# Optimization experiments

Measured on AMD Instinct MI355X. Metric: run time of the kernel, lower is better.

Reference implementation:

```python
import jax, jax.numpy as jnp
import numpy as np

PI = 3.1415926
MAX_V = 8  # max vertices of a quad-quad convex intersection
ALPHA, GAMMA, IOU_THRES = 0.25, 2.0, 0.5


def xyxy2xywh_a(b):
    cx = (b[..., 0] + b[..., 2]) * 0.5
    cy = (b[..., 1] + b[..., 3]) * 0.5
    w = b[..., 2] - b[..., 0]
    h = b[..., 3] - b[..., 1]
    return jnp.stack([cx, cy, w, h, b[..., 4]], -1)


def rbox_2_quad(b):
    # [N,5] (x1,y1,x2,y2,theta_deg) -> [N,4,2] corner quads
    x = xyxy2xywh_a(b)
    cx, cy, w, h, t = x[:, 0], x[:, 1], x[:, 2], x[:, 3], x[:, 4]
    th = t * (PI / 180.0)
    c, s = jnp.cos(th), jnp.sin(th)
    dx = jnp.array([-0.5, 0.5, 0.5, -0.5], b.dtype)
    dy = jnp.array([-0.5, -0.5, 0.5, 0.5], b.dtype)
    px = cx[:, None] + dx * w[:, None] * c[:, None] - dy * h[:, None] * s[:, None]
    py = cy[:, None] + dx * w[:, None] * s[:, None] + dy * h[:, None] * c[:, None]
    return jnp.stack([px, py], -1)


def min_area_square(b):
    cx = (b[:, 0] + b[:, 2]) * 0.5
    cy = (b[:, 1] + b[:, 3]) * 0.5
    s = jnp.maximum(b[:, 2] - b[:, 0], b[:, 3] - b[:, 1]) * 0.5
    return jnp.stack([cx - s, cy - s, cx + s, cy + s], 1)


def bbox_overlaps(a, b):
    # axis-aligned IoU matrix [N,M]
    lt = jnp.maximum(a[:, None, :2], b[None, :, :2])
    rb = jnp.minimum(a[:, None, 2:], b[None, :, 2:])
    wh = jnp.clip(rb - lt, 0.0)
    inter = wh[..., 0] * wh[..., 1]
    area_a = (a[:, 2] - a[:, 0]) * (a[:, 3] - a[:, 1])
    area_b = (b[:, 2] - b[:, 0]) * (b[:, 3] - b[:, 1])
    return inter / (area_a[:, None] + area_b[None, :] - inter + 1e-6)


def points_in_quads(pts, quads):
    # pointsJf: pts [A,2] inside convex quads [G,4,2] -> [A,G] {0,1}
    e = jnp.roll(quads, -1, axis=1) - quads  # [G,4,2]
    rel = pts[:, None, None, :] - quads[None]  # [A,G,4,2]
    cr = e[None, ..., 0] * rel[..., 1] - e[None, ..., 1] * rel[..., 0]
    inside = jnp.all(cr >= 0, -1) | jnp.all(cr <= 0, -1)
    return inside.astype(pts.dtype)


def _signed_area2(q):
    return jnp.sum(q[:, 0] * jnp.roll(q[:, 1], -1) - jnp.roll(q[:, 0], -1) * q[:, 1])


def _quad_inter_area(q1, q2):
    # Sutherland-Hodgman clipping of quad q1 by convex quad q2, fixed 8-vertex buffer
    q1 = jnp.where(_signed_area2(q1) < 0, q1[::-1], q1)
    q2 = jnp.where(_signed_area2(q2) < 0, q2[::-1], q2)
    poly = jnp.zeros((MAX_V, 2), q1.dtype).at[:4].set(q1)
    edges = jnp.stack([q2, jnp.roll(q2, -1, axis=0)], 1)  # [4,2,2]

    def clip(carry, edge):
        poly, n = carry
        a, b = edge[0], edge[1]
        idx = jnp.arange(MAX_V)
        nidx = jnp.where(idx + 1 < n, idx + 1, 0)
        cur, nxt = poly, poly[nidx]
        d = b - a
        dc = d[0] * (cur[:, 1] - a[1]) - d[1] * (cur[:, 0] - a[0])
        dn = d[0] * (nxt[:, 1] - a[1]) - d[1] * (nxt[:, 0] - a[0])
        denom = dc - dn
        t = dc / jnp.where(jnp.abs(denom) < 1e-12, 1e-12, denom)
        inter = cur + t[:, None] * (nxt - cur)
        active = idx < n
        keep_cur = active & (dc >= 0)
        keep_int = active & ((dc >= 0) != (dn >= 0))
        pts = jnp.stack([cur, inter], 1).reshape(2 * MAX_V, 2)
        flags = jnp.stack([keep_cur, keep_int], 1).reshape(-1)
        pos = jnp.where(flags, jnp.cumsum(flags) - 1, MAX_V)
        newpoly = jnp.zeros((MAX_V + 1, 2), poly.dtype).at[pos].set(pts)[:MAX_V]
        return (newpoly, flags.sum()), None

    (poly, n), _ = jax.lax.scan(clip, (poly, jnp.int32(4)), edges)
    idx = jnp.arange(MAX_V)
    nidx = jnp.where(idx + 1 < n, idx + 1, 0)
    contrib = poly[:, 0] * poly[nidx, 1] - poly[nidx, 0] * poly[:, 1]
    area = 0.5 * jnp.abs(jnp.sum(jnp.where(idx < n, contrib, 0.0)))
    return jnp.where(n >= 3, area, 0.0)


def rbox_overlaps(quads_a, quads_g, gate, thresh=0.1):
    area_a = 0.5 * jnp.abs(jax.vmap(_signed_area2)(quads_a))
    area_g = 0.5 * jnp.abs(jax.vmap(_signed_area2)(quads_g))
    inter = jax.vmap(lambda qa: jax.vmap(lambda qg: _quad_inter_area(qa, qg))(quads_g))(quads_a)
    iou = inter / (area_a[:, None] + area_g[None, :] - inter + 1e-6)
    return jnp.where(gate > thresh, iou, 0.0)


def encode(anchors, gt):
    a = xyxy2xywh_a(anchors)
    g = xyxy2xywh_a(gt)
    dx = (g[:, 0] - a[:, 0]) / a[:, 2]
    dy = (g[:, 1] - a[:, 1]) / a[:, 3]
    dw = jnp.log(g[:, 2] / a[:, 2])
    dh = jnp.log(g[:, 3] / a[:, 3])
    dt = (g[:, 4] - a[:, 4]) * (PI / 180.0)
    return jnp.stack([dx, dy, dw, dh, dt], 1)


def decode(anchors, deltas):
    a = xyxy2xywh_a(anchors)
    cx = a[..., 0] + deltas[..., 0] * a[..., 2]
    cy = a[..., 1] + deltas[..., 1] * a[..., 3]
    w = a[..., 2] * jnp.exp(deltas[..., 2])
    h = a[..., 3] * jnp.exp(deltas[..., 3])
    t = a[..., 4] + deltas[..., 4] * (180.0 / PI)
    return jnp.stack([cx, cy, w, h, t], -1)


def smooth_l1(x, t, beta=1.0 / 9):
    diff = jnp.abs(x - t)
    return jnp.where(diff < beta, 0.5 * diff * diff / beta, diff - 0.5 * beta)


def _forward(classifications, regressions, anchors, annotations):
    B = classifications.shape[0]
    _ = decode(anchors, regressions)  # all_pred_boxes (unused when func='smooth')
    cls_losses, reg_losses = [], []
    for j in range(B):
        cls = jnp.clip(classifications[j], 1e-4, 1.0 - 1e-4)
        anch = anchors[j]
        gtb = annotations[j, :, :5]
        labels = annotations[j, :, 5].astype(jnp.int32)
        indicator = bbox_overlaps(min_area_square(anch), min_area_square(gtb))
        centers = xyxy2xywh_a(anch)[:, :2]
        quads_g = rbox_2_quad(gtb)
        inside = points_in_quads(centers, quads_g)
        quads_a = rbox_2_quad(anch)
        ious = rbox_overlaps(quads_a, quads_g, inside * indicator)  # [A,G]
        iou_max = ious.max(1)
        iou_argmax = ious.argmax(1)
        pos = iou_max >= IOU_THRES
        max_gt = ious.max(0)
        argmax_gt = ious.argmax(0)
        low = (max_gt < IOU_THRES).astype(jnp.int32)
        pos = (pos.astype(jnp.int32).at[argmax_gt].max(low)).astype(bool)
        num_pos = pos.sum()
        C = cls.shape[1]
        onehot = jax.nn.one_hot(labels[iou_argmax], C, dtype=cls.dtype)
        tgt = -jnp.ones_like(cls)
        tgt = jnp.where((iou_max < IOU_THRES - 0.1)[:, None], 0.0, tgt)
        tgt = jnp.where(pos[:, None], onehot, tgt)
        af = jnp.where(tgt == 1.0, ALPHA, 1.0 - ALPHA)
        fw = af * jnp.where(tgt == 1.0, 1.0 - cls, cls) ** GAMMA
        bce = -(tgt * jnp.log(cls + 1e-6) + (1.0 - tgt) * jnp.log(1.0 - cls + 1e-6))
        cls_loss = jnp.where(tgt != -1.0, fw * bce, 0.0).sum() / jnp.maximum(num_pos.astype(cls.dtype), 1.0)
        cls_losses.append(cls_loss)
        reg_t = encode(anch, gtb[iou_argmax])
        l = smooth_l1(regressions[j], reg_t)
        denom = (jnp.maximum(num_pos, 1) * l.shape[1]).astype(l.dtype)
        reg_loss = jnp.where(num_pos > 0, (l * pos[:, None].astype(l.dtype)).sum() / denom, 0.0)
        reg_losses.append(reg_loss)
    loss_cls = 5.0 * jnp.stack(cls_losses).mean(keepdims=True)
    loss_reg = 2.0 * jnp.stack(reg_losses).mean(keepdims=True)
    return loss_cls, loss_reg


def setup_inputs() -> dict:
    key = jax.random.key(0)
    ks = jax.random.split(key, 8)
    B, A, G, C = 2, 32768, 32, 15
    cls = jax.random.uniform(ks[0], (B, A, C), jnp.float32)
    reg = jax.random.normal(ks[1], (B, A, 5), jnp.float32) * 0.1
    ac = jax.random.uniform(ks[2], (B, A, 2), jnp.float32, 0.0, 1024.0)
    awh = jax.random.uniform(ks[3], (B, A, 2), jnp.float32, 16.0, 256.0)
    anchors = jnp.concatenate([ac - awh * 0.5, ac + awh * 0.5, jnp.zeros((B, A, 1), jnp.float32)], -1)
    gc = jax.random.uniform(ks[4], (B, G, 2), jnp.float32, 64.0, 960.0)
    gwh = jax.random.uniform(ks[5], (B, G, 2), jnp.float32, 24.0, 300.0)
    gt = jax.random.uniform(ks[6], (B, G, 1), jnp.float32, -90.0, 90.0)
    glab = jax.random.randint(ks[7], (B, G, 1), 0, C).astype(jnp.float32)
    annotations = jnp.concatenate([gc - gwh * 0.5, gc + gwh * 0.5, gt, glab], -1)
    return {"classifications": cls, "regressions": reg, "anchors": anchors, "annotations": annotations}


def reference(classifications, regressions, anchors, annotations):
    return _forward(classifications, regressions, anchors, annotations)
```

## Files before the change

### kernel.cpp

```cpp
#include <hip/hip_runtime.h>

#define A_N 32768
#define G_N 32
#define C_N 15
#define BPB 128
#define DEG2RAD ((float)(3.1415926 / 180.0))
#define BETA (1.0f / 9.0f)

typedef unsigned long long ull;

template <int NIN>
__device__ __forceinline__ int clip_pass(float ax, float ay, float dx, float dy,
                                         float (&PX)[8], float (&PY)[8], int n) {
  constexpr int NOUT = (NIN + 1 < 8) ? NIN + 1 : 8;
  float d[NIN];
#pragma unroll
  for (int i = 0; i < NIN; ++i)
    d[i] = dx * (PY[i] - ay) - dy * (PX[i] - ax);
  float NX[NOUT], NY[NOUT];
#pragma unroll
  for (int i = 0; i < NOUT; ++i) { NX[i] = 0.f; NY[i] = 0.f; }
  int m = 0;
#pragma unroll
  for (int i = 0; i < NIN; ++i) {
    if (i < n) {
      bool w = (i + 1 < n);
      float dn = w ? d[(i + 1) % NIN] : d[0];
      float xn = w ? PX[(i + 1) % NIN] : PX[0];
      float yn = w ? PY[(i + 1) % NIN] : PY[0];
      bool kc = (d[i] >= 0.f);
      bool kn = (dn >= 0.f);
      if (kc) {
#pragma unroll
        for (int o = 0; o < NOUT; ++o)
          if (o <= 2 * i && m == o) { NX[o] = PX[i]; NY[o] = PY[i]; }
        ++m;
      }
      if (kc != kn) {
        float den = d[i] - dn;
        if (fabsf(den) < 1e-12f) den = 1e-12f;
        float t = d[i] / den;
        float ix = PX[i] + t * (xn - PX[i]);
        float iy = PY[i] + t * (yn - PY[i]);
#pragma unroll
        for (int o = 0; o < NOUT; ++o)
          if (o <= 2 * i + 1 && m == o) { NX[o] = ix; NY[o] = iy; }
        ++m;
      }
    }
  }
#pragma unroll
  for (int i = 0; i < NOUT; ++i) { PX[i] = NX[i]; PY[i] = NY[i]; }
#pragma unroll
  for (int i = NOUT; i < 8; ++i) { PX[i] = 0.f; PY[i] = 0.f; }
  return m;
}

__global__ __launch_bounds__(256) void k_fused(
    const float* __restrict__ cls_in, const float* __restrict__ reg_in,
    const float* __restrict__ anchors, const float* __restrict__ annot,
    ull* __restrict__ gpart, ull* __restrict__ rowpack,
    float* __restrict__ cls_part, float* __restrict__ reg_part,
    int* __restrict__ cnt_part) {
  int j = blockIdx.x >> 7;
  int blk = blockIdx.x & (BPB - 1);
  int tid = threadIdx.x;
  int a = blk * 256 + tid;
  size_t ia = (size_t)j * A_N + a;

  __shared__ float4 g_sqv[G_N];
  __shared__ float2 g_meta[G_N];
  __shared__ float4 g_vx[G_N], g_vy[G_N];
  __shared__ float4 a_qx[256], a_qy[256];
  __shared__ float a_area[256];
  __shared__ ull rowbest[256];
  __shared__ ull colmax[G_N];
  __shared__ unsigned short list[256 * G_N];
  __shared__ int cnt;
  __shared__ int lab[G_N];
  __shared__ float gcx[G_N], gcy[G_N], gw2[G_N], gh2[G_N], gth[G_N];
  __shared__ float w1[4], w2[4];
  __shared__ int w3[4];

  float pcv[C_N];
  {
    const float* c = cls_in + ia * C_N;
#pragma unroll
    for (int ci = 0; ci < C_N; ++ci) pcv[ci] = c[ci];
  }
  float rv[5];
  {
    const float* r = reg_in + ia * 5;
#pragma unroll
    for (int i = 0; i < 5; ++i) rv[i] = r[i];
  }

  if (tid == 0) cnt = 0;
  rowbest[tid] = 0xFFFFFFFFull;
  if (tid < G_N) colmax[tid] = 0xFFFFFFFFull;

  if (tid < G_N) {
    const float* g = annot + ((size_t)j * G_N + tid) * 6;
    float x1 = g[0], y1 = g[1], x2 = g[2], y2 = g[3], t = g[4];
    float cxx = (x1 + x2) * 0.5f, cyy = (y1 + y2) * 0.5f;
    float w = x2 - x1, h = y2 - y1;
    gcx[tid] = cxx; gcy[tid] = cyy; gw2[tid] = w; gh2[tid] = h; gth[tid] = t;
    lab[tid] = (int)g[5];
    float th = t * DEG2RAD;
    float c = cosf(th), s = sinf(th);
    const float ddx[4] = {-0.5f, 0.5f, 0.5f, -0.5f};
    const float ddy[4] = {-0.5f, -0.5f, 0.5f, 0.5f};
    float px[4], py[4];
#pragma unroll
    for (int k = 0; k < 4; ++k) {
      px[k] = cxx + ddx[k] * w * c - ddy[k] * h * s;
      py[k] = cyy + ddx[k] * w * s + ddy[k] * h * c;
    }
    float s2 = 0.f;
#pragma unroll
    for (int k = 0; k < 4; ++k)
      s2 += px[k] * py[(k + 1) & 3] - px[(k + 1) & 3] * py[k];
    if (s2 < 0.f) {
      g_vx[tid] = make_float4(px[3], px[2], px[1], px[0]);
      g_vy[tid] = make_float4(py[3], py[2], py[1], py[0]);
    } else {
      g_vx[tid] = make_float4(px[0], px[1], px[2], px[3]);
      g_vy[tid] = make_float4(py[0], py[1], py[2], py[3]);
    }
    float half = fmaxf(w, h) * 0.5f;
    float sx1 = cxx - half, sy1 = cyy - half, sx2 = cxx + half, sy2 = cyy + half;
    g_sqv[tid] = make_float4(sx1, sy1, sx2, sy2);
    g_meta[tid] = make_float2((sx2 - sx1) * (sy2 - sy1), 0.5f * fabsf(s2));
  }

  const float* an = anchors + ia * 5;
  float ax1 = an[0], ay1 = an[1], ax2 = an[2], ay2 = an[3], at = an[4];
  float acx = (ax1 + ax2) * 0.5f, acy = (ay1 + ay2) * 0.5f;
  float aw = ax2 - ax1, ah = ay2 - ay1;
  float ath = at * DEG2RAD;
  float ac = cosf(ath), asn = sinf(ath);
  {
    const float ddx[4] = {-0.5f, 0.5f, 0.5f, -0.5f};
    const float ddy[4] = {-0.5f, -0.5f, 0.5f, 0.5f};
    float apx[4], apy[4];
#pragma unroll
    for (int k = 0; k < 4; ++k) {
      apx[k] = acx + ddx[k] * aw * ac - ddy[k] * ah * asn;
      apy[k] = acy + ddx[k] * aw * asn + ddy[k] * ah * ac;
    }
    float s2a = 0.f;
#pragma unroll
    for (int k = 0; k < 4; ++k)
      s2a += apx[k] * apy[(k + 1) & 3] - apx[(k + 1) & 3] * apy[k];
    if (s2a < 0.f) {
      float tx = apx[0], ty = apy[0];
      apx[0] = apx[3]; apy[0] = apy[3]; apx[3] = tx; apy[3] = ty;
      tx = apx[1]; ty = apy[1];
      apx[1] = apx[2]; apy[1] = apy[2]; apx[2] = tx; apy[2] = ty;
    }
    a_qx[tid] = make_float4(apx[0], apx[1], apx[2], apx[3]);
    a_qy[tid] = make_float4(apy[0], apy[1], apy[2], apy[3]);
    a_area[tid] = 0.5f * fabsf(s2a);
  }
  float half = fmaxf(aw, ah) * 0.5f;
  float asx1 = acx - half, asy1 = acy - half, asx2 = acx + half, asy2 = acy + half;
  float asarea = (asx2 - asx1) * (asy2 - asy1);
  __syncthreads();

#pragma unroll 2
  for (int g = 0; g < G_N; ++g) {
    float4 sq = g_sqv[g];
    float2 meta = g_meta[g];
    float ltx = fmaxf(asx1, sq.x);
    float lty = fmaxf(asy1, sq.y);
    float rbx = fminf(asx2, sq.z);
    float rby = fminf(asy2, sq.w);
    float iw = fmaxf(rbx - ltx, 0.f);
    float ih = fmaxf(rby - lty, 0.f);
    float inter_s = iw * ih;
    float ind = inter_s / (asarea + meta.x - inter_s + 1e-6f);
    float4 vx = g_vx[g], vy = g_vy[g];
    float cr0 = (vx.y - vx.x) * (acy - vy.x) - (vy.y - vy.x) * (acx - vx.x);
    float cr1 = (vx.z - vx.y) * (acy - vy.y) - (vy.z - vy.y) * (acx - vx.y);
    float cr2 = (vx.w - vx.z) * (acy - vy.z) - (vy.w - vy.z) * (acx - vx.z);
    float cr3 = (vx.x - vx.w) * (acy - vy.w) - (vy.x - vy.w) * (acx - vx.w);
    bool pall = (cr0 >= 0.f) & (cr1 >= 0.f) & (cr2 >= 0.f) & (cr3 >= 0.f);
    bool nall = (cr0 <= 0.f) & (cr1 <= 0.f) & (cr2 <= 0.f) & (cr3 <= 0.f);
    if ((pall || nall) && ind > 0.1f) {
      int p = atomicAdd(&cnt, 1);
      list[p] = (unsigned short)((tid << 5) | g);
    }
  }
  __syncthreads();

  int np = cnt;
  for (int i = tid; i < np; i += 256) {
    int ent = list[i];
    int la = ent >> 5, g = ent & 31;
    float4 aqx = a_qx[la], aqy = a_qy[la];
    float PX[8], PY[8];
    PX[0] = aqx.x; PX[1] = aqx.y; PX[2] = aqx.z; PX[3] = aqx.w;
    PY[0] = aqy.x; PY[1] = aqy.y; PY[2] = aqy.z; PY[3] = aqy.w;
#pragma unroll
    for (int k = 4; k < 8; ++k) { PX[k] = 0.f; PY[k] = 0.f; }
    float4 gvx = g_vx[g], gvy = g_vy[g];
    int n = 4;
    n = clip_pass<4>(gvx.x, gvy.x, gvx.y - gvx.x, gvy.y - gvy.x, PX, PY, n);
    n = clip_pass<5>(gvx.y, gvy.y, gvx.z - gvx.y, gvy.z - gvy.y, PX, PY, n);
    n = clip_pass<6>(gvx.z, gvy.z, gvx.w - gvx.z, gvy.w - gvy.z, PX, PY, n);
    n = clip_pass<7>(gvx.w, gvy.w, gvx.x - gvx.w, gvy.x - gvy.w, PX, PY, n);
    float s = 0.f;
#pragma unroll
    for (int k = 0; k < 8; ++k) {
      if (k < n) {
        float xn = (k + 1 < n) ? PX[(k + 1) & 7] : PX[0];
        float yn = (k + 1 < n) ? PY[(k + 1) & 7] : PY[0];
        s += PX[k] * yn - xn * PY[k];
      }
    }
    float inter = (n >= 3) ? 0.5f * fabsf(s) : 0.f;
    float v = inter / (a_area[la] + g_meta[g].y - inter + 1e-6f);
    ull pr = ((ull)__float_as_uint(v) << 32) | (unsigned)(~(unsigned)g);
    atomicMax(&rowbest[la], pr);
    unsigned ga = (unsigned)(blk * 256 + la);
    ull pc = ((ull)__float_as_uint(v) << 32) | (unsigned)(~ga);
    atomicMax(&colmax[g], pc);
  }
  __syncthreads();

  ull rb = rowbest[tid];
  float im = __uint_as_float((unsigned)(rb >> 32));
  int arg = (int)(~(unsigned)rb);
  int p = (im >= 0.5f) ? 1 : 0;

  rowpack[ia] = rb;
  if (tid < G_N)
    gpart[((size_t)j * BPB + blk) * G_N + tid] = colmax[tid];

  int lb = lab[arg];
  float csum = 0.f;
  bool bg = (im < 0.4f);
  if (p || bg) {
#pragma unroll
    for (int ci = 0; ci < C_N; ++ci) {
      float pc = fminf(fmaxf(pcv[ci], 1e-4f), 0.9999f);
      bool tgt1 = p && (ci == lb);
      if (tgt1)
        csum += 0.25f * (1.f - pc) * (1.f - pc) * (-__logf(pc + 1e-6f));
      else
        csum += 0.75f * pc * pc * (-__logf(1.f - pc + 1e-6f));
    }
  }

  float rsum = 0.f;
  if (p) {
    float t5[5];
    t5[0] = (gcx[arg] - acx) / aw;
    t5[1] = (gcy[arg] - acy) / ah;
    t5[2] = __logf(gw2[arg] / aw);
    t5[3] = __logf(gh2[arg] / ah);
    t5[4] = (gth[arg] - at) * DEG2RAD;
#pragma unroll
    for (int i = 0; i < 5; ++i) {
      float d = fabsf(rv[i] - t5[i]);
      rsum += (d < BETA) ? (0.5f * d * d / BETA) : (d - 0.5f * BETA);
    }
  }

  float v1 = csum, v2 = rsum;
  int v3 = p;
#pragma unroll
  for (int off = 32; off; off >>= 1) {
    v1 += __shfl_xor(v1, off);
    v2 += __shfl_xor(v2, off);
    v3 += __shfl_xor(v3, off);
  }
  int wv = tid >> 6, ln = tid & 63;
  if (ln == 0) { w1[wv] = v1; w2[wv] = v2; w3[wv] = v3; }
  __syncthreads();
  if (tid == 0) {
    cls_part[blockIdx.x] = (w1[0] + w1[1]) + (w1[2] + w1[3]);
    reg_part[blockIdx.x] = (w2[0] + w2[1]) + (w2[2] + w2[3]);
    cnt_part[blockIdx.x] = (w3[0] + w3[1]) + (w3[2] + w3[3]);
  }
}

__global__ __launch_bounds__(256) void k_fix(
    const float* __restrict__ cls_in, const float* __restrict__ reg_in,
    const float* __restrict__ anchors, const float* __restrict__ annot,
    const ull* __restrict__ gpart, const ull* __restrict__ rowpack,
    const float* __restrict__ cls_part, const float* __restrict__ reg_part,
    const int* __restrict__ cnt_part, float* __restrict__ out, int B) {
  int tid = threadIdx.x;
  __shared__ ull sred[8][G_N];
  __shared__ int fanchor[G_N], owner[G_N];
  __shared__ float dcs[G_N], drs[G_N];
  __shared__ int dct[G_N];
  __shared__ float bd_c[8], bd_r[8];
  __shared__ int bd_n[8];
  __shared__ float s1[256], s2[256];
  __shared__ int s3[256];

  for (int j = 0; j < B; ++j) {
    {
      int g = tid & 31, chunk = tid >> 5;
      const ull* gp = gpart + (size_t)j * BPB * G_N;
      ull m = 0;
#pragma unroll
      for (int b = 0; b < BPB / 8; ++b) {
        ull v = gp[(size_t)(chunk * (BPB / 8) + b) * G_N + g];
        m = v > m ? v : m;
      }
      sred[chunk][g] = m;
    }
    __syncthreads();
    if (tid < G_N) {
      ull m = sred[0][tid];
#pragma unroll
      for (int c = 1; c < 8; ++c) m = sred[c][tid] > m ? sred[c][tid] : m;
      float v = __uint_as_float((unsigned)(m >> 32));
      fanchor[tid] = (v < 0.5f) ? (int)(~(unsigned)m) : -1;
      dcs[tid] = 0.f; drs[tid] = 0.f; dct[tid] = 0;
      owner[tid] = 0;
    }
    __syncthreads();
    if (tid == 0) {
      for (int g = 0; g < G_N; ++g) {
        int af = fanchor[g];
        if (af < 0) continue;
        bool dup = false;
        for (int g2 = 0; g2 < g; ++g2) dup = dup || (fanchor[g2] == af);
        owner[g] = dup ? 0 : 1;
      }
    }
    __syncthreads();
    if (tid < G_N && owner[tid]) {
      int af = fanchor[tid];
      size_t ia = (size_t)j * A_N + af;
      ull rb = rowpack[ia];
      float im = __uint_as_float((unsigned)(rb >> 32));
      if (im < 0.5f) {
        int arg = (int)(~(unsigned)rb);
        const float* gg = annot + ((size_t)j * G_N + arg) * 6;
        int lb = (int)gg[5];
        const float* c = cls_in + ia * C_N;
        bool bg = (im < 0.4f);
        float ca = 0.f, cb = 0.f;
#pragma unroll
        for (int ci = 0; ci < C_N; ++ci) {
          float pc = fminf(fmaxf(c[ci], 1e-4f), 0.9999f);
          float neg = 0.75f * pc * pc * (-__logf(1.f - pc + 1e-6f));
          if (ci == lb)
            ca += 0.25f * (1.f - pc) * (1.f - pc) * (-__logf(pc + 1e-6f));
          else
            ca += neg;
          if (bg) cb += neg;
        }
        const float* an = anchors + ia * 5;
        float acx = (an[0] + an[2]) * 0.5f, acy = (an[1] + an[3]) * 0.5f;
        float aw = an[2] - an[0], ah = an[3] - an[1];
        float gcxv = (gg[0] + gg[2]) * 0.5f, gcyv = (gg[1] + gg[3]) * 0.5f;
        float gwv = gg[2] - gg[0], ghv = gg[3] - gg[1];
        const float* r = reg_in + ia * 5;
        float t5[5];
        t5[0] = (gcxv - acx) / aw;
        t5[1] = (gcyv - acy) / ah;
        t5[2] = __logf(gwv / aw);
        t5[3] = __logf(ghv / ah);
        t5[4] = (gg[4] - an[4]) * DEG2RAD;
        float rs = 0.f;
#pragma unroll
        for (int i = 0; i < 5; ++i) {
          float d = fabsf(r[i] - t5[i]);
          rs += (d < BETA) ? (0.5f * d * d / BETA) : (d - 0.5f * BETA);
        }
        dcs[tid] = ca - cb;
        drs[tid] = rs;
        dct[tid] = 1;
      }
    }
    __syncthreads();
    if (tid == 0) {
      float dc = 0.f, dr = 0.f;
      int dn = 0;
      for (int g = 0; g < G_N; ++g) { dc += dcs[g]; dr += drs[g]; dn += dct[g]; }
      bd_c[j] = dc; bd_r[j] = dr; bd_n[j] = dn;
    }
    __syncthreads();
  }

  int P = B * BPB;
  float cv = 0.f, rvv = 0.f;
  int nv = 0;
  if (tid < P) { cv = cls_part[tid]; rvv = reg_part[tid]; nv = cnt_part[tid]; }
  s1[tid] = cv; s2[tid] = rvv; s3[tid] = nv;
  __syncthreads();
  for (int o = 64; o; o >>= 1) {
    if ((tid & 127) < o) {
      s1[tid] += s1[tid + o]; s2[tid] += s2[tid + o]; s3[tid] += s3[tid + o];
    }
    __syncthreads();
  }
  if (tid == 0) {
    float cl = 0.f, rl = 0.f;
    for (int jj = 0; jj < B; ++jj) {
      float cs = s1[jj * 128] + bd_c[jj];
      float rs = s2[jj * 128] + bd_r[jj];
      int np = s3[jj * 128] + bd_n[jj];
      float npf = (np > 0) ? (float)np : 1.f;
      cl += cs / npf;
      rl += (np > 0) ? rs / (npf * 5.f) : 0.f;
    }
    out[0] = 5.0f * cl / (float)B;
    out[1] = 2.0f * rl / (float)B;
  }
}

extern "C" void kernel_launch(void* const* d_in, const int* in_sizes, int n_in,
                              void* d_out, int out_size, void* d_ws, size_t ws_size,
                              hipStream_t stream) {
  const float* cls = (const float*)d_in[0];
  const float* reg = (const float*)d_in[1];
  const float* anc = (const float*)d_in[2];
  const float* ann = (const float*)d_in[3];
  int B = in_sizes[3] / (G_N * 6);

  char* w = (char*)d_ws;
  ull* gpart = (ull*)w;        w += (size_t)B * BPB * G_N * sizeof(ull);
  ull* rowpack = (ull*)w;      w += (size_t)B * A_N * sizeof(ull);
  float* cls_part = (float*)w; w += (size_t)B * BPB * 4;
  float* reg_part = (float*)w; w += (size_t)B * BPB * 4;
  int* cnt_part = (int*)w;     w += (size_t)B * BPB * 4;

  k_fused<<<B * BPB, 256, 0, stream>>>(cls, reg, anc, ann, gpart, rowpack,
                                       cls_part, reg_part, cnt_part);
  k_fix<<<1, 256, 0, stream>>>(cls, reg, anc, ann, gpart, rowpack,
                               cls_part, reg_part, cnt_part, (float*)d_out, B);
}
```

Measured before the change: 41.25 us.

## Split each anchor's GT scan and class loss across four threads per anchor

The fused kernel now launches 1024 threads per block, with four threads per anchor. Each thread scans a quarter of the ground-truth boxes in the candidate filter and handles up to four of the class logits in the focal loss. Only one of the four threads writes the anchor quad, rowpack and regression loss. The goal is more parallelism and shorter per-thread serial loops with only 256 blocks in the grid. In exchange, the anchor-setup work is computed redundantly by all four threads, the blocks are much larger, and pressure on the shared-memory atomics rises.

```diff
diff --git a/kernel.cpp b/kernel.cpp
--- a/kernel.cpp
+++ b/kernel.cpp
@@ -3,7 +3,9 @@
 #define A_N 32768
 #define G_N 32
 #define C_N 15
-#define BPB 128
+#define APB 256
+#define H_N 4
+#define BPB (A_N / APB)
 #define DEG2RAD ((float)(3.1415926 / 180.0))
 #define BETA (1.0f / 9.0f)
 
@@ -56,7 +58,7 @@
   return m;
 }
 
-__global__ __launch_bounds__(256) void k_fused(
+__global__ __launch_bounds__(1024) void k_fused(
     const float* __restrict__ cls_in, const float* __restrict__ reg_in,
     const float* __restrict__ anchors, const float* __restrict__ annot,
     ull* __restrict__ gpart, ull* __restrict__ rowpack,
@@ -65,46 +67,54 @@
   int j = blockIdx.x >> 7;
   int blk = blockIdx.x & (BPB - 1);
   int tid = threadIdx.x;
-  int a = blk * 256 + tid;
+  int la = tid & (APB - 1);
+  int h = tid >> 8;
+  int a = blk * APB + la;
   size_t ia = (size_t)j * A_N + a;
 
   __shared__ float4 g_sqv[G_N];
   __shared__ float2 g_meta[G_N];
   __shared__ float4 g_vx[G_N], g_vy[G_N];
-  __shared__ float4 a_qx[256], a_qy[256];
-  __shared__ float a_area[256];
-  __shared__ ull rowbest[256];
+  __shared__ float4 a_qx[APB], a_qy[APB];
+  __shared__ float a_area[APB];
+  __shared__ ull rowbest[APB];
   __shared__ ull colmax[G_N];
-  __shared__ unsigned short list[256 * G_N];
+  __shared__ unsigned short list[APB * G_N];
   __shared__ int cnt;
   __shared__ int lab[G_N];
   __shared__ float gcx[G_N], gcy[G_N], gw2[G_N], gh2[G_N], gth[G_N];
-  __shared__ float w1[4], w2[4];
-  __shared__ int w3[4];
-
-  float pcv[C_N];
+  __shared__ float w1[16], w2[16];
+  __shared__ int w3[16];
+
+  float pcv[4];
   {
     const float* c = cls_in + ia * C_N;
 #pragma unroll
-    for (int ci = 0; ci < C_N; ++ci) pcv[ci] = c[ci];
-  }
-  float rv[5];
-  {
+    for (int k = 0; k < 4; ++k) {
+      int ci = h * 4 + k;
+      pcv[k] = (ci < C_N) ? c[ci] : 0.f;
+    }
+  }
+  float rvv[5];
+  if (h == 0) {
     const float* r = reg_in + ia * 5;
 #pragma unroll
-    for (int i = 0; i < 5; ++i) rv[i] = r[i];
+    for (int i = 0; i < 5; ++i) rvv[i] = r[i];
+  } else {
+#pragma unroll
+    for (int i = 0; i < 5; ++i) rvv[i] = 0.f;
   }
 
   if (tid == 0) cnt = 0;
-  rowbest[tid] = 0xFFFFFFFFull;
+  if (tid < APB) rowbest[tid] = 0xFFFFFFFFull;
   if (tid < G_N) colmax[tid] = 0xFFFFFFFFull;
 
   if (tid < G_N) {
     const float* g = annot + ((size_t)j * G_N + tid) * 6;
     float x1 = g[0], y1 = g[1], x2 = g[2], y2 = g[3], t = g[4];
     float cxx = (x1 + x2) * 0.5f, cyy = (y1 + y2) * 0.5f;
-    float w = x2 - x1, h = y2 - y1;
-    gcx[tid] = cxx; gcy[tid] = cyy; gw2[tid] = w; gh2[tid] = h; gth[tid] = t;
+    float w = x2 - x1, hh = y2 - y1;
+    gcx[tid] = cxx; gcy[tid] = cyy; gw2[tid] = w; gh2[tid] = hh; gth[tid] = t;
     lab[tid] = (int)g[5];
     float th = t * DEG2RAD;
     float c = cosf(th), s = sinf(th);
@@ -113,8 +123,8 @@
     float px[4], py[4];
 #pragma unroll
     for (int k = 0; k < 4; ++k) {
-      px[k] = cxx + ddx[k] * w * c - ddy[k] * h * s;
-      py[k] = cyy + ddx[k] * w * s + ddy[k] * h * c;
+      px[k] = cxx + ddx[k] * w * c - ddy[k] * hh * s;
+      py[k] = cyy + ddx[k] * w * s + ddy[k] * hh * c;
     }
     float s2 = 0.f;
 #pragma unroll
@@ -127,7 +137,7 @@
       g_vx[tid] = make_float4(px[0], px[1], px[2], px[3]);
       g_vy[tid] = make_float4(py[0], py[1], py[2], py[3]);
     }
-    float half = fmaxf(w, h) * 0.5f;
+    float half = fmaxf(w, hh) * 0.5f;
     float sx1 = cxx - half, sy1 = cyy - half, sx2 = cxx + half, sy2 = cyy + half;
     g_sqv[tid] = make_float4(sx1, sy1, sx2, sy2);
     g_meta[tid] = make_float2((sx2 - sx1) * (sy2 - sy1), 0.5f * fabsf(s2));
@@ -158,17 +168,20 @@
       tx = apx[1]; ty = apy[1];
       apx[1] = apx[2]; apy[1] = apy[2]; apx[2] = tx; apy[2] = ty;
     }
-    a_qx[tid] = make_float4(apx[0], apx[1], apx[2], apx[3]);
-    a_qy[tid] = make_float4(apy[0], apy[1], apy[2], apy[3]);
-    a_area[tid] = 0.5f * fabsf(s2a);
+    if (h == 0) {
+      a_qx[la] = make_float4(apx[0], apx[1], apx[2], apx[3]);
+      a_qy[la] = make_float4(apy[0], apy[1], apy[2], apy[3]);
+      a_area[la] = 0.5f * fabsf(s2a);
+    }
   }
   float half = fmaxf(aw, ah) * 0.5f;
   float asx1 = acx - half, asy1 = acy - half, asx2 = acx + half, asy2 = acy + half;
   float asarea = (asx2 - asx1) * (asy2 - asy1);
   __syncthreads();
 
-#pragma unroll 2
-  for (int g = 0; g < G_N; ++g) {
+#pragma unroll
+  for (int gg = 0; gg < G_N / H_N; ++gg) {
+    int g = h * (G_N / H_N) + gg;
     float4 sq = g_sqv[g];
     float2 meta = g_meta[g];
     float ltx = fmaxf(asx1, sq.x);
@@ -188,16 +201,16 @@
     bool nall = (cr0 <= 0.f) & (cr1 <= 0.f) & (cr2 <= 0.f) & (cr3 <= 0.f);
     if ((pall || nall) && ind > 0.1f) {
       int p = atomicAdd(&cnt, 1);
-      list[p] = (unsigned short)((tid << 5) | g);
+      list[p] = (unsigned short)((la << 5) | g);
     }
   }
   __syncthreads();
 
   int np = cnt;
-  for (int i = tid; i < np; i += 256) {
+  for (int i = tid; i < np; i += 1024) {
     int ent = list[i];
-    int la = ent >> 5, g = ent & 31;
-    float4 aqx = a_qx[la], aqy = a_qy[la];
+    int ca = ent >> 5, g = ent & 31;
+    float4 aqx = a_qx[ca], aqy = a_qy[ca];
     float PX[8], PY[8];
     PX[0] = aqx.x; PX[1] = aqx.y; PX[2] = aqx.z; PX[3] = aqx.w;
     PY[0] = aqy.x; PY[1] = aqy.y; PY[2] = aqy.z; PY[3] = aqy.w;
@@ -219,21 +232,21 @@
       }
     }
     float inter = (n >= 3) ? 0.5f * fabsf(s) : 0.f;
-    float v = inter / (a_area[la] + g_meta[g].y - inter + 1e-6f);
+    float v = inter / (a_area[ca] + g_meta[g].y - inter + 1e-6f);
     ull pr = ((ull)__float_as_uint(v) << 32) | (unsigned)(~(unsigned)g);
-    atomicMax(&rowbest[la], pr);
-    unsigned ga = (unsigned)(blk * 256 + la);
+    atomicMax(&rowbest[ca], pr);
+    unsigned ga = (unsigned)(blk * APB + ca);
     ull pc = ((ull)__float_as_uint(v) << 32) | (unsigned)(~ga);
     atomicMax(&colmax[g], pc);
   }
   __syncthreads();
 
-  ull rb = rowbest[tid];
+  ull rb = rowbest[la];
   float im = __uint_as_float((unsigned)(rb >> 32));
   int arg = (int)(~(unsigned)rb);
   int p = (im >= 0.5f) ? 1 : 0;
 
-  rowpack[ia] = rb;
+  if (h == 0) rowpack[ia] = rb;
   if (tid < G_N)
     gpart[((size_t)j * BPB + blk) * G_N + tid] = colmax[tid];
 
@@ -242,18 +255,21 @@
   bool bg = (im < 0.4f);
   if (p || bg) {
 #pragma unroll
-    for (int ci = 0; ci < C_N; ++ci) {
-      float pc = fminf(fmaxf(pcv[ci], 1e-4f), 0.9999f);
-      bool tgt1 = p && (ci == lb);
-      if (tgt1)
-        csum += 0.25f * (1.f - pc) * (1.f - pc) * (-__logf(pc + 1e-6f));
-      else
-        csum += 0.75f * pc * pc * (-__logf(1.f - pc + 1e-6f));
+    for (int k = 0; k < 4; ++k) {
+      int ci = h * 4 + k;
+      if (ci < C_N) {
+        float pc = fminf(fmaxf(pcv[k], 1e-4f), 0.9999f);
+        bool tgt1 = p && (ci == lb);
+        if (tgt1)
+          csum += 0.25f * (1.f - pc) * (1.f - pc) * (-__logf(pc + 1e-6f));
+        else
+          csum += 0.75f * pc * pc * (-__logf(1.f - pc + 1e-6f));
+      }
     }
   }
 
   float rsum = 0.f;
-  if (p) {
+  if (p && h == 0) {
     float t5[5];
     t5[0] = (gcx[arg] - acx) / aw;
     t5[1] = (gcy[arg] - acy) / ah;
@@ -262,13 +278,14 @@
     t5[4] = (gth[arg] - at) * DEG2RAD;
 #pragma unroll
     for (int i = 0; i < 5; ++i) {
-      float d = fabsf(rv[i] - t5[i]);
+      float d = fabsf(rvv[i] - t5[i]);
       rsum += (d < BETA) ? (0.5f * d * d / BETA) : (d - 0.5f * BETA);
     }
   }
+  int pcnt = (h == 0) ? p : 0;
 
   float v1 = csum, v2 = rsum;
-  int v3 = p;
+  int v3 = pcnt;
 #pragma unroll
   for (int off = 32; off; off >>= 1) {
     v1 += __shfl_xor(v1, off);
@@ -279,9 +296,13 @@
   if (ln == 0) { w1[wv] = v1; w2[wv] = v2; w3[wv] = v3; }
   __syncthreads();
   if (tid == 0) {
-    cls_part[blockIdx.x] = (w1[0] + w1[1]) + (w1[2] + w1[3]);
-    reg_part[blockIdx.x] = (w2[0] + w2[1]) + (w2[2] + w2[3]);
-    cnt_part[blockIdx.x] = (w3[0] + w3[1]) + (w3[2] + w3[3]);
+    float t1 = 0.f, t2 = 0.f;
+    int t3 = 0;
+#pragma unroll
+    for (int k = 0; k < 16; ++k) { t1 += w1[k]; t2 += w2[k]; t3 += w3[k]; }
+    cls_part[blockIdx.x] = t1;
+    reg_part[blockIdx.x] = t2;
+    cnt_part[blockIdx.x] = t3;
   }
 }
 
@@ -432,8 +453,8 @@
   float* reg_part = (float*)w; w += (size_t)B * BPB * 4;
   int* cnt_part = (int*)w;     w += (size_t)B * BPB * 4;
 
-  k_fused<<<B * BPB, 256, 0, stream>>>(cls, reg, anc, ann, gpart, rowpack,
-                                       cls_part, reg_part, cnt_part);
+  k_fused<<<B * BPB, 1024, 0, stream>>>(cls, reg, anc, ann, gpart, rowpack,
+                                        cls_part, reg_part, cnt_part);
   k_fix<<<1, 256, 0, stream>>>(cls, reg, anc, ann, gpart, rowpack,
                                cls_part, reg_part, cnt_part, (float*)d_out, B);
 }
```

New measurement: 35.82 us. -13.2%, faster.
